# Optimization experiments

Measured on AMD Instinct MI355X. Metric: run time of the kernel, lower is better.

## Reference

```python
import jax, jax.numpy as jnp
import numpy as np

D_MODEL, H, D_FF = 512, 8, 2048
B, S = 2, 2048
EPS = 1e-6


def _layernorm(x, alpha, beta):
    # Faithful to the torch module: unbiased std (ddof=1), eps added to STD,
    # scalar alpha/beta parameters.
    m = jnp.mean(x, axis=-1, keepdims=True)
    var = jnp.sum((x - m) ** 2, axis=-1, keepdims=True) / (x.shape[-1] - 1)
    std = jnp.sqrt(var)
    return alpha * (x - m) / (std + EPS) + beta


def _mha(x, mask, Wq, bq, Wk, bk, Wv, bv, Wo, bo):
    Bn, Sn, D = x.shape
    dk = D // H
    q = (x @ Wq + bq).reshape(Bn, Sn, H, dk).transpose(0, 2, 1, 3)  # [B,H,S,dk]
    k = (x @ Wk + bk).reshape(Bn, Sn, H, dk).transpose(0, 2, 1, 3)
    v = (x @ Wv + bv).reshape(Bn, Sn, H, dk).transpose(0, 2, 1, 3)
    scores = jnp.einsum('bhqd,bhkd->bhqk', q, k) / jnp.sqrt(jnp.float32(dk))
    scores = jnp.where(mask == 0, -jnp.inf, scores)  # mask [B,1,1,S] broadcasts
    attn = jax.nn.softmax(scores, axis=-1)
    out = jnp.einsum('bhqk,bhkd->bhqd', attn, v)
    out = out.transpose(0, 2, 1, 3).reshape(Bn, Sn, D)
    return out @ Wo + bo


def _ffn(x, W1, b1, W2, b2):
    return jax.nn.relu(x @ W1 + b1) @ W2 + b2


def setup_inputs() -> dict:
    key = jax.random.key(0)
    ks = jax.random.split(key, 12)
    sd = 1.0 / np.sqrt(D_MODEL)
    sdf = 1.0 / np.sqrt(D_FF)
    inp = {
        'x': jax.random.normal(ks[0], (B, S, D_MODEL), jnp.float32),
        'src_mask': jnp.ones((B, 1, 1, S), jnp.int32),
        'Wq': jax.random.normal(ks[1], (D_MODEL, D_MODEL), jnp.float32) * sd,
        'bq': jnp.zeros((D_MODEL,), jnp.float32),
        'Wk': jax.random.normal(ks[2], (D_MODEL, D_MODEL), jnp.float32) * sd,
        'bk': jnp.zeros((D_MODEL,), jnp.float32),
        'Wv': jax.random.normal(ks[3], (D_MODEL, D_MODEL), jnp.float32) * sd,
        'bv': jnp.zeros((D_MODEL,), jnp.float32),
        'Wo': jax.random.normal(ks[4], (D_MODEL, D_MODEL), jnp.float32) * sd,
        'bo': jnp.zeros((D_MODEL,), jnp.float32),
        'W1': jax.random.normal(ks[5], (D_MODEL, D_FF), jnp.float32) * sd,
        'b1': jnp.zeros((D_FF,), jnp.float32),
        'W2': jax.random.normal(ks[6], (D_FF, D_MODEL), jnp.float32) * sdf,
        'b2': jnp.zeros((D_MODEL,), jnp.float32),
        'alpha1': jnp.ones((1,), jnp.float32),
        'beta1': jnp.zeros((1,), jnp.float32),
        'alpha2': jnp.ones((1,), jnp.float32),
        'beta2': jnp.zeros((1,), jnp.float32),
    }
    return inp


def reference(x, src_mask, Wq, bq, Wk, bk, Wv, bv, Wo, bo,
              W1, b1, W2, b2, alpha1, beta1, alpha2, beta2):
    # SkipConnection 0: x + dropout(MHA(LN(x)))  (dropout=0 -> identity)
    h1 = _layernorm(x, alpha1, beta1)
    x = x + _mha(h1, src_mask, Wq, bq, Wk, bk, Wv, bv, Wo, bo)
    # SkipConnection 1: x + dropout(FFN(LN(x)))
    h2 = _layernorm(x, alpha2, beta2)
    x = x + _ffn(h2, W1, b1, W2, b2)
    return x
```

## Files before the change

### kernel.cpp

```cpp
#include <hip/hip_runtime.h>
#include <hip/hip_bf16.h>

typedef __hip_bfloat16 bf16;
typedef __attribute__((ext_vector_type(8))) short s8v;
typedef __attribute__((ext_vector_type(4))) float f32x4;

#define DM 512
#define NH 8
#define DKH 64
#define DFF 2048
#define NB 2
#define NS 2048
#define NR (NB*NS)
#define LN_EPS 1e-6f
#define NEG_BIG (-1e30f)
#define LDQKV (3*DM)
#define SM_SCALE2 0.18033688f
#define SM_SHIFT2 (-8.656170245f)
#define PART_ELEMS (NB*NH*NS*DKH)

#define MFMA_B16(a,b,c) __builtin_amdgcn_mfma_f32_16x16x32_bf16(a,b,c,0,0,0)

#define GLOAD16(g, l) __builtin_amdgcn_global_load_lds( \
    (const __attribute__((address_space(1))) void*)(g), \
    (__attribute__((address_space(3))) void*)(l), 16, 0, 0)

__device__ __forceinline__ float us2f(unsigned int u){ return __uint_as_float(u << 16); }
__device__ __forceinline__ float b2f(bf16 v){ return __bfloat162float(v); }
__device__ __forceinline__ float ldf(const float* p){ return *p; }
__device__ __forceinline__ float ldf(const bf16* p){ return __bfloat162float(*p); }
__device__ __forceinline__ void stf(float* p, float v){ *p = v; }
__device__ __forceinline__ void stf(bf16* p, float v){ *p = __float2bfloat16(v); }

__device__ __forceinline__ int swz(int row, int colbyte){
  return ((row<<7) + colbyte) ^ ((row&7)<<4);
}

__device__ __forceinline__ float wsum(float v){
#pragma unroll
  for(int o=32;o>0;o>>=1) v += __shfl_down(v,o,64);
  return v;
}

__device__ __forceinline__ void stage_tile(char* lds, const bf16* g, int ld, int R, int tid){
  int wave = tid>>6, lane = tid&63;
  int nch = R*8;
  for(int c0 = wave*64; c0 < nch; c0 += 256){
    int c = c0 + lane;
    int row = c>>3;
    int blk = (c&7) ^ (row&7);
    GLOAD16(g + (size_t)row*ld + blk*8, lds + c0*16);
  }
}
__device__ __forceinline__ s8v read_frag(const char* lds, int row, int col){
  return *reinterpret_cast<const s8v*>(lds + swz(row, col<<1));
}

template<typename TI>
__global__ __launch_bounds__(256) void ln_kernel(const TI* __restrict__ x,
    bf16* __restrict__ out, const float* __restrict__ ap, const float* __restrict__ bp){
  __shared__ float s1[4], s2[4];
  int row = blockIdx.x, tid = threadIdx.x;
  const TI* xr = x + (size_t)row*DM;
  float v0 = ldf(xr+tid), v1 = ldf(xr+tid+256);
  float s = wsum(v0+v1);
  float q = wsum(v0*v0+v1*v1);
  int wid = tid>>6, lane = tid&63;
  if(lane==0){ s1[wid]=s; s2[wid]=q; }
  __syncthreads();
  float S = s1[0]+s1[1]+s1[2]+s1[3];
  float Q = s2[0]+s2[1]+s2[2]+s2[3];
  float mean = S*(1.f/DM);
  float var  = (Q - (float)DM*mean*mean)*(1.f/(DM-1));
  float sd   = sqrtf(fmaxf(var,0.f));
  float sc = (*ap)/(sd+LN_EPS);
  float b = *bp;
  bf16* orow = out + (size_t)row*DM;
  orow[tid]     = __float2bfloat16((v0-mean)*sc + b);
  orow[tid+256] = __float2bfloat16((v1-mean)*sc + b);
}

__global__ __launch_bounds__(256) void transpose_all(
    const float* __restrict__ Wq, const float* __restrict__ Wk,
    const float* __restrict__ Wv, const float* __restrict__ Wo,
    const float* __restrict__ W1, const float* __restrict__ W2,
    bf16* __restrict__ WTqkv, bf16* __restrict__ WTo,
    bf16* __restrict__ WT1, bf16* __restrict__ WT2){
  __shared__ float t[64][65];
  int tb = blockIdx.x;
  const float* W; bf16* WT; int K, N, nx;
  if(tb < 192){
    int w = tb>>6; tb &= 63;
    W = (w==0)?Wq:(w==1)?Wk:Wv; WT = WTqkv + w*512*512; K=512; N=512; nx=8;
  } else if(tb < 256){ tb -= 192; W=Wo; WT=WTo; K=512; N=512; nx=8; }
  else if(tb < 512){ tb -= 256; W=W1; WT=WT1; K=512; N=2048; nx=32; }
  else { tb -= 512; W=W2; WT=WT2; K=2048; N=512; nx=8; }
  int n0 = (tb % nx)*64, k0 = (tb / nx)*64;
  int tid = threadIdx.x;
  int rr = tid>>6, cc = tid&63;
#pragma unroll
  for(int r=rr;r<64;r+=4) t[r][cc] = W[(size_t)(k0+r)*N + n0+cc];
  __syncthreads();
#pragma unroll
  for(int r=rr;r<64;r+=4) WT[(size_t)(n0+r)*K + k0+cc] = __float2bfloat16(t[cc][r]);
}

__global__ __launch_bounds__(256) void transpose_v(const bf16* __restrict__ Vg,
    bf16* __restrict__ VT){
  __shared__ float t[64][65];
  int tid = threadIdx.x;
  int s0 = blockIdx.x*64; int bh = blockIdx.y;
  int b = bh>>3, h = bh&7;
  int rr = tid>>6, cc = tid&63;
#pragma unroll
  for(int r=rr;r<64;r+=4)
    t[r][cc] = b2f(Vg[((size_t)(b*NS + s0+r))*LDQKV + h*DKH + cc]);
  __syncthreads();
#pragma unroll
  for(int r=rr;r<64;r+=4)
    VT[((size_t)bh*DKH + r)*NS + s0+cc] = __float2bfloat16(t[cc][r]);
}

template<int BM, int BN, int DBUF, int RELU, int QKVSEL, typename TR, typename TO>
__global__ __launch_bounds__(256) void mfma_gemm(
    const bf16* __restrict__ A, const bf16* __restrict__ WT,
    const float* __restrict__ bias0, const float* __restrict__ bias1,
    const float* __restrict__ bias2,
    const TR* __restrict__ resid, TO* __restrict__ out, int M, int N, int K){
  constexpr int NW = BN/2, NF = NW/16, MI = BM/32, WRS = BM/2;
  __shared__ char lA[1+DBUF][BM*128];
  __shared__ char lB[1+DBUF][BN*128];
  int tid = threadIdx.x, wave = tid>>6, lane = tid&63;
  int m0 = blockIdx.x*BM, n0 = blockIdx.y*BN;
  int wr = wave>>1, wc = wave&1;
  int g = lane>>4, li = lane&15;
  f32x4 acc[MI][NF] = {};
  if(DBUF){
    stage_tile(lA[0], A + (size_t)m0*K, K, BM, tid);
    stage_tile(lB[0], WT + (size_t)n0*K, K, BN, tid);
    __syncthreads();
  }
  int cur = 0;
  for(int kt=0; kt<K; kt+=64, cur^=DBUF){
    if(!DBUF){
      stage_tile(lA[0], A + (size_t)m0*K + kt, K, BM, tid);
      stage_tile(lB[0], WT + (size_t)n0*K + kt, K, BN, tid);
      __syncthreads();
    } else if(kt+64 < K){
      stage_tile(lA[cur^1], A + (size_t)m0*K + kt+64, K, BM, tid);
      stage_tile(lB[cur^1], WT + (size_t)n0*K + kt+64, K, BN, tid);
    }
#pragma unroll
    for(int kk=0; kk<2; kk++){
      s8v af[MI], bfr[NF];
#pragma unroll
      for(int mi=0;mi<MI;mi++) af[mi] = read_frag(lA[cur], wr*WRS+mi*16+li, kk*32+g*8);
#pragma unroll
      for(int ni=0;ni<NF;ni++) bfr[ni] = read_frag(lB[cur], wc*NW+ni*16+li, kk*32+g*8);
#pragma unroll
      for(int mi=0;mi<MI;mi++)
#pragma unroll
        for(int ni=0;ni<NF;ni++)
          acc[mi][ni] = MFMA_B16(af[mi], bfr[ni], acc[mi][ni]);
    }
    __syncthreads();
  }
#pragma unroll
  for(int mi=0;mi<MI;mi++)
#pragma unroll
  for(int ni=0;ni<NF;ni++){
    int row = m0 + wr*WRS + mi*16 + g*4;
    int col = n0 + wc*NW + ni*16 + li;
    const float* bp = bias0;
    if(QKVSEL) bp = (col<512)? bias0 : (col<1024)? (bias1-512) : (bias2-1024);
    float bb = bp[col];
#pragma unroll
    for(int r=0;r<4;r++){
      float v = acc[mi][ni][r] + bb;
      if(RELU) v = fmaxf(v, 0.f);
      size_t off = (size_t)(row+r)*N + col;
      if(resid) v += ldf(resid+off);
      stf(out+off, v);
    }
  }
}

__global__ __launch_bounds__(256,4) void flash_attn(
    const bf16* __restrict__ QKV, const bf16* __restrict__ VT,
    const int* __restrict__ mask, bf16* __restrict__ partA,
    bf16* __restrict__ partB, float* __restrict__ lbuf){
  __shared__ char lK[2][64*128];
  __shared__ char lV[2][64*128];
  __shared__ char lP[4][16*128];
  int tid = threadIdx.x, wave = tid>>6, lane = tid&63;
  int q0 = blockIdx.x*64, h = blockIdx.y;
  int b = blockIdx.z>>1, kh = blockIdx.z&1;
  int kbase = kh*(NS/2);
  int g = lane>>4, li = lane&15;
  const bf16* Qg  = QKV + ((size_t)b*NS + q0)*LDQKV + h*DKH;
  const bf16* Kg  = QKV + ((size_t)b*NS + kbase)*LDQKV + DM + h*DKH;
  const bf16* VTg = VT + ((size_t)(b*NH + h))*DKH*NS + kbase;
  stage_tile(lK[0], Qg, LDQKV, 64, tid);
  __syncthreads();
  s8v qf0 = read_frag(lK[0], wave*16+li, g*8);
  s8v qf1 = read_frag(lK[0], wave*16+li, 32+g*8);
  __syncthreads();
  stage_tile(lK[0], Kg, LDQKV, 64, tid);
  stage_tile(lV[0], VTg, NS, 64, tid);
  unsigned long long mb = 0;
#pragma unroll 16
  for(int j=0;j<64;j++)
    mb |= (unsigned long long)(mask[b*NS + kbase + j*16 + li] != 0) << j;
  __syncthreads();
  f32x4 acc[4] = {};
  f32x4 acc_l = {};
  s8v ones;
#pragma unroll
  for(int j=0;j<8;j++) ones[j] = (short)0x3F80;
  char* lPw = lP[wave];
  int cur = 0;
  for(int kt=0; kt<NS/2; kt+=64, cur^=1){
    if(kt+64 < NS/2){
      stage_tile(lK[cur^1], Kg + (size_t)(kt+64)*LDQKV, LDQKV, 64, tid);
      stage_tile(lV[cur^1], VTg + kt+64, NS, 64, tid);
    }
    f32x4 S[4] = {};
#pragma unroll
    for(int kk=0;kk<2;kk++){
      s8v qf = kk ? qf1 : qf0;
      s8v kf[4];
#pragma unroll
      for(int ni=0;ni<4;ni++) kf[ni] = read_frag(lK[cur], ni*16+li, kk*32+g*8);
#pragma unroll
      for(int ni=0;ni<4;ni++)
        S[ni] = MFMA_B16(qf, kf[ni], S[ni]);
    }
    int jb = kt>>4;
    float madd[4];
#pragma unroll
    for(int ni=0;ni<4;ni++)
      madd[ni] = ((mb>>(jb+ni))&1ull) ? SM_SHIFT2 : NEG_BIG;
#pragma unroll
    for(int r=0;r<4;r++){
      float e0 = exp2f(fminf(fmaf(S[0][r], SM_SCALE2, madd[0]), 80.f));
      float e1 = exp2f(fminf(fmaf(S[1][r], SM_SCALE2, madd[1]), 80.f));
      float e2 = exp2f(fminf(fmaf(S[2][r], SM_SCALE2, madd[2]), 80.f));
      float e3 = exp2f(fminf(fmaf(S[3][r], SM_SCALE2, madd[3]), 80.f));
      int row = g*4 + r;
      *reinterpret_cast<bf16*>(lPw + swz(row, (0*16+li)<<1)) = __float2bfloat16(e0);
      *reinterpret_cast<bf16*>(lPw + swz(row, (1*16+li)<<1)) = __float2bfloat16(e1);
      *reinterpret_cast<bf16*>(lPw + swz(row, (2*16+li)<<1)) = __float2bfloat16(e2);
      *reinterpret_cast<bf16*>(lPw + swz(row, (3*16+li)<<1)) = __float2bfloat16(e3);
    }
#pragma unroll
    for(int kk=0;kk<2;kk++){
      s8v pf = read_frag(lPw, li, kk*32+g*8);
      s8v vf[4];
#pragma unroll
      for(int nd=0;nd<4;nd++) vf[nd] = read_frag(lV[cur], nd*16+li, kk*32+g*8);
#pragma unroll
      for(int nd=0;nd<4;nd++)
        acc[nd] = MFMA_B16(pf, vf[nd], acc[nd]);
      acc_l = MFMA_B16(pf, ones, acc_l);
    }
    __syncthreads();
  }
  bf16* part = kh ? partB : partA;
  size_t qb = (size_t)(b*NH + h)*NS;
#pragma unroll
  for(int r=0;r<4;r++){
    int qrow = q0 + wave*16 + g*4 + r;
#pragma unroll
    for(int nd=0;nd<4;nd++)
      part[(qb + qrow)*DKH + nd*16 + li] = __float2bfloat16(acc[nd][r]);
    if(li==0)
      lbuf[((size_t)((b*NH+h)*2 + kh))*NS + qrow] = acc_l[r];
  }
}

__global__ __launch_bounds__(256) void combine_attn(const bf16* __restrict__ pA,
    const bf16* __restrict__ pB, const float* __restrict__ lbuf,
    bf16* __restrict__ cx){
  int e = blockIdx.x*256 + threadIdx.x;
  int idx = e*4;
  int d = idx & 63, q = (idx>>6)&(NS-1), h = (idx>>17)&7, b = idx>>20;
  uint2 ua = *reinterpret_cast<const uint2*>(pA+idx);
  uint2 ub = *reinterpret_cast<const uint2*>(pB+idx);
  float lA = lbuf[((size_t)((b*NH+h)*2+0))*NS + q];
  float lB = lbuf[((size_t)((b*NH+h)*2+1))*NS + q];
  float il = 1.f/(lA+lB);
  bf16* o = cx + ((size_t)(b*NS+q)*DM + h*DKH + d);
  o[0] = __float2bfloat16((us2f(ua.x&0xffffu)+us2f(ub.x&0xffffu))*il);
  o[1] = __float2bfloat16((us2f(ua.x>>16)+us2f(ub.x>>16))*il);
  o[2] = __float2bfloat16((us2f(ua.y&0xffffu)+us2f(ub.y&0xffffu))*il);
  o[3] = __float2bfloat16((us2f(ua.y>>16)+us2f(ub.y>>16))*il);
}

extern "C" void kernel_launch(void* const* d_in, const int* in_sizes, int n_in,
                              void* d_out, int out_size, void* d_ws, size_t ws_size,
                              hipStream_t stream){
  const float* x   = (const float*)d_in[0];
  const int* mask  = (const int*)d_in[1];
  const float* Wq = (const float*)d_in[2];
  const float* bq = (const float*)d_in[3];
  const float* Wk = (const float*)d_in[4];
  const float* bk = (const float*)d_in[5];
  const float* Wv = (const float*)d_in[6];
  const float* bv = (const float*)d_in[7];
  const float* Wo = (const float*)d_in[8];
  const float* bo = (const float*)d_in[9];
  const float* W1 = (const float*)d_in[10];
  const float* b1 = (const float*)d_in[11];
  const float* W2 = (const float*)d_in[12];
  const float* b2 = (const float*)d_in[13];
  const float* a1 = (const float*)d_in[14];
  const float* be1= (const float*)d_in[15];
  const float* a2 = (const float*)d_in[16];
  const float* be2= (const float*)d_in[17];

  char* ws = (char*)d_ws;
  bf16* h1    = (bf16*)(ws);
  bf16* accA  = (bf16*)(ws);
  bf16* WTqkv = (bf16*)(ws + (size_t)( 4<<20));
  bf16* WTo   = (bf16*)(ws + (size_t)(11<<19));
  bf16* WT1   = (bf16*)(ws + (size_t)( 8<<20));
  bf16* WT2   = (bf16*)(ws + (size_t)(10<<20));
  bf16* qkv   = (bf16*)(ws + (size_t)(12<<20));
  bf16* VT    = (bf16*)(ws + (size_t)(24<<20));
  bf16* cx    = (bf16*)(ws + (size_t)(24<<20));
  bf16* x1    = h1;
  bf16* h2    = (bf16*)(ws + (size_t)( 4<<20));
  bf16* mid   = qkv;
  float* lbuf = (float*)d_out;
  bf16* accB  = (bf16*)((char*)d_out + (1<<20));

  transpose_all<<<768,256,0,stream>>>(Wq,Wk,Wv,Wo,W1,W2, WTqkv,WTo,WT1,WT2);

  ln_kernel<float><<<NR,256,0,stream>>>(x, h1, a1, be1);
  mfma_gemm<128,64,1,0,1,float,bf16><<<dim3(32,24),256,0,stream>>>(
      h1, WTqkv, bq, bk, bv, (const float*)nullptr, qkv, NR, LDQKV, DM);
  transpose_v<<<dim3(32,16),256,0,stream>>>(qkv + 2*DM, VT);
  flash_attn<<<dim3(NS/64,NH,NB*2),256,0,stream>>>(qkv, VT, mask, accA, accB, lbuf);
  combine_attn<<<PART_ELEMS/1024,256,0,stream>>>(accA, accB, lbuf, cx);
  mfma_gemm<64,64,1,0,0,float,bf16><<<dim3(64,8),256,0,stream>>>(
      cx, WTo, bo, bo, bo, x, x1, NR, DM, DM);
  ln_kernel<bf16><<<NR,256,0,stream>>>(x1, h2, a2, be2);
  mfma_gemm<128,128,0,1,0,float,bf16><<<dim3(32,16),256,0,stream>>>(
      h2, WT1, b1, b1, b1, (const float*)nullptr, mid, NR, DFF, DM);
  mfma_gemm<64,64,1,0,0,bf16,float><<<dim3(64,8),256,0,stream>>>(
      mid, WT2, b2, b2, b2, x1, (float*)d_out, NR, DM, DFF);
}
```

Baseline: 145.5 us.

## Drop split-K attention and LDS staging; load K/V fragments directly from global

The flash attention kernel no longer splits keys into two halves. It handles all 2048 keys per block and normalizes its output in place, which removes the combine kernel and the partial-output buffers. K and V fragments are read straight from global memory into registers instead of through double-buffered LDS with barriers. The QKV GEMM tile changes to 128x128, and the Wo transpose moves into a separate small kernel so its workspace can be reused. The kernel now has half as many blocks, each with a longer serial loop, and direct global fragment loads may have worse coalescing and more latency exposure. The overflow clamp on exp2 is also removed, which is only safe while the scores stay small.

```diff
diff --git a/kernel.cpp b/kernel.cpp
--- a/kernel.cpp
+++ b/kernel.cpp
@@ -17,7 +17,6 @@
 #define LDQKV (3*DM)
 #define SM_SCALE2 0.18033688f
 #define SM_SHIFT2 (-8.656170245f)
-#define PART_ELEMS (NB*NH*NS*DKH)
 
 #define MFMA_B16(a,b,c) __builtin_amdgcn_mfma_f32_16x16x32_bf16(a,b,c,0,0,0)
 
@@ -25,7 +24,6 @@
     (const __attribute__((address_space(1))) void*)(g), \
     (__attribute__((address_space(3))) void*)(l), 16, 0, 0)
 
-__device__ __forceinline__ float us2f(unsigned int u){ return __uint_as_float(u << 16); }
 __device__ __forceinline__ float b2f(bf16 v){ return __bfloat162float(v); }
 __device__ __forceinline__ float ldf(const float* p){ return *p; }
 __device__ __forceinline__ float ldf(const bf16* p){ return __bfloat162float(*p); }
@@ -82,21 +80,32 @@
 
 __global__ __launch_bounds__(256) void transpose_all(
     const float* __restrict__ Wq, const float* __restrict__ Wk,
-    const float* __restrict__ Wv, const float* __restrict__ Wo,
-    const float* __restrict__ W1, const float* __restrict__ W2,
-    bf16* __restrict__ WTqkv, bf16* __restrict__ WTo,
-    bf16* __restrict__ WT1, bf16* __restrict__ WT2){
+    const float* __restrict__ Wv, const float* __restrict__ W1,
+    const float* __restrict__ W2,
+    bf16* __restrict__ WTqkv, bf16* __restrict__ WT1, bf16* __restrict__ WT2){
   __shared__ float t[64][65];
   int tb = blockIdx.x;
   const float* W; bf16* WT; int K, N, nx;
   if(tb < 192){
     int w = tb>>6; tb &= 63;
     W = (w==0)?Wq:(w==1)?Wk:Wv; WT = WTqkv + w*512*512; K=512; N=512; nx=8;
-  } else if(tb < 256){ tb -= 192; W=Wo; WT=WTo; K=512; N=512; nx=8; }
-  else if(tb < 512){ tb -= 256; W=W1; WT=WT1; K=512; N=2048; nx=32; }
-  else { tb -= 512; W=W2; WT=WT2; K=2048; N=512; nx=8; }
+  } else if(tb < 448){ tb -= 192; W=W1; WT=WT1; K=512; N=2048; nx=32; }
+  else { tb -= 448; W=W2; WT=WT2; K=2048; N=512; nx=8; }
   int n0 = (tb % nx)*64, k0 = (tb / nx)*64;
   int tid = threadIdx.x;
+  int rr = tid>>6, cc = tid&63;
+#pragma unroll
+  for(int r=rr;r<64;r+=4) t[r][cc] = W[(size_t)(k0+r)*N + n0+cc];
+  __syncthreads();
+#pragma unroll
+  for(int r=rr;r<64;r+=4) WT[(size_t)(n0+r)*K + k0+cc] = __float2bfloat16(t[cc][r]);
+}
+
+__global__ __launch_bounds__(256) void transpose_w(const float* __restrict__ W,
+    bf16* __restrict__ WT, int K, int N){
+  __shared__ float t[64][65];
+  int tid = threadIdx.x;
+  int n0 = blockIdx.x*64, k0 = blockIdx.y*64;
   int rr = tid>>6, cc = tid&63;
 #pragma unroll
   for(int r=rr;r<64;r+=4) t[r][cc] = W[(size_t)(k0+r)*N + n0+cc];
@@ -185,67 +194,66 @@
   }
 }
 
-__global__ __launch_bounds__(256,4) void flash_attn(
+__global__ __launch_bounds__(256,3) void flash_attn(
     const bf16* __restrict__ QKV, const bf16* __restrict__ VT,
-    const int* __restrict__ mask, bf16* __restrict__ partA,
-    bf16* __restrict__ partB, float* __restrict__ lbuf){
-  __shared__ char lK[2][64*128];
-  __shared__ char lV[2][64*128];
+    const int* __restrict__ mask, bf16* __restrict__ O){
   __shared__ char lP[4][16*128];
   int tid = threadIdx.x, wave = tid>>6, lane = tid&63;
-  int q0 = blockIdx.x*64, h = blockIdx.y;
-  int b = blockIdx.z>>1, kh = blockIdx.z&1;
-  int kbase = kh*(NS/2);
+  int q0 = blockIdx.x*64, h = blockIdx.y, b = blockIdx.z;
   int g = lane>>4, li = lane&15;
   const bf16* Qg  = QKV + ((size_t)b*NS + q0)*LDQKV + h*DKH;
-  const bf16* Kg  = QKV + ((size_t)b*NS + kbase)*LDQKV + DM + h*DKH;
-  const bf16* VTg = VT + ((size_t)(b*NH + h))*DKH*NS + kbase;
-  stage_tile(lK[0], Qg, LDQKV, 64, tid);
-  __syncthreads();
-  s8v qf0 = read_frag(lK[0], wave*16+li, g*8);
-  s8v qf1 = read_frag(lK[0], wave*16+li, 32+g*8);
-  __syncthreads();
-  stage_tile(lK[0], Kg, LDQKV, 64, tid);
-  stage_tile(lV[0], VTg, NS, 64, tid);
-  unsigned long long mb = 0;
+  const bf16* Kl  = QKV + (size_t)b*NS*LDQKV + DM + h*DKH + (size_t)li*LDQKV + g*8;
+  const bf16* Vl  = VT + ((size_t)(b*NH + h))*DKH*NS + (size_t)li*NS + g*8;
+  s8v qf0 = *reinterpret_cast<const s8v*>(Qg + (size_t)(wave*16+li)*LDQKV + g*8);
+  s8v qf1 = *reinterpret_cast<const s8v*>(Qg + (size_t)(wave*16+li)*LDQKV + 32 + g*8);
+  unsigned long long mb0 = 0, mb1 = 0;
 #pragma unroll 16
   for(int j=0;j<64;j++)
-    mb |= (unsigned long long)(mask[b*NS + kbase + j*16 + li] != 0) << j;
-  __syncthreads();
+    mb0 |= (unsigned long long)(mask[b*NS + j*16 + li] != 0) << j;
+#pragma unroll 16
+  for(int j=0;j<64;j++)
+    mb1 |= (unsigned long long)(mask[b*NS + 1024 + j*16 + li] != 0) << j;
   f32x4 acc[4] = {};
   f32x4 acc_l = {};
   s8v ones;
 #pragma unroll
   for(int j=0;j<8;j++) ones[j] = (short)0x3F80;
   char* lPw = lP[wave];
-  int cur = 0;
-  for(int kt=0; kt<NS/2; kt+=64, cur^=1){
-    if(kt+64 < NS/2){
-      stage_tile(lK[cur^1], Kg + (size_t)(kt+64)*LDQKV, LDQKV, 64, tid);
-      stage_tile(lV[cur^1], VTg + kt+64, NS, 64, tid);
-    }
+  for(int kt=0; kt<NS; kt+=64){
+    const bf16* Kt = Kl + (size_t)kt*LDQKV;
+    s8v kf[2][4], vf[2][4];
+#pragma unroll
+    for(int kk=0;kk<2;kk++)
+#pragma unroll
+      for(int ni=0;ni<4;ni++)
+        kf[kk][ni] = *reinterpret_cast<const s8v*>(Kt + (size_t)(ni*16)*LDQKV + kk*32);
+#pragma unroll
+    for(int kk=0;kk<2;kk++)
+#pragma unroll
+      for(int nd=0;nd<4;nd++)
+        vf[kk][nd] = *reinterpret_cast<const s8v*>(Vl + (size_t)(nd*16)*NS + kt + kk*32);
     f32x4 S[4] = {};
 #pragma unroll
     for(int kk=0;kk<2;kk++){
       s8v qf = kk ? qf1 : qf0;
-      s8v kf[4];
-#pragma unroll
-      for(int ni=0;ni<4;ni++) kf[ni] = read_frag(lK[cur], ni*16+li, kk*32+g*8);
 #pragma unroll
       for(int ni=0;ni<4;ni++)
-        S[ni] = MFMA_B16(qf, kf[ni], S[ni]);
+        S[ni] = MFMA_B16(qf, kf[kk][ni], S[ni]);
     }
     int jb = kt>>4;
     float madd[4];
 #pragma unroll
-    for(int ni=0;ni<4;ni++)
-      madd[ni] = ((mb>>(jb+ni))&1ull) ? SM_SHIFT2 : NEG_BIG;
+    for(int ni=0;ni<4;ni++){
+      int j = jb + ni;
+      unsigned long long w = (j & 64) ? mb1 : mb0;
+      madd[ni] = ((w>>(j&63))&1ull) ? SM_SHIFT2 : NEG_BIG;
+    }
 #pragma unroll
     for(int r=0;r<4;r++){
-      float e0 = exp2f(fminf(fmaf(S[0][r], SM_SCALE2, madd[0]), 80.f));
-      float e1 = exp2f(fminf(fmaf(S[1][r], SM_SCALE2, madd[1]), 80.f));
-      float e2 = exp2f(fminf(fmaf(S[2][r], SM_SCALE2, madd[2]), 80.f));
-      float e3 = exp2f(fminf(fmaf(S[3][r], SM_SCALE2, madd[3]), 80.f));
+      float e0 = exp2f(fmaf(S[0][r], SM_SCALE2, madd[0]));
+      float e1 = exp2f(fmaf(S[1][r], SM_SCALE2, madd[1]));
+      float e2 = exp2f(fmaf(S[2][r], SM_SCALE2, madd[2]));
+      float e3 = exp2f(fmaf(S[3][r], SM_SCALE2, madd[3]));
       int row = g*4 + r;
       *reinterpret_cast<bf16*>(lPw + swz(row, (0*16+li)<<1)) = __float2bfloat16(e0);
       *reinterpret_cast<bf16*>(lPw + swz(row, (1*16+li)<<1)) = __float2bfloat16(e1);
@@ -255,45 +263,21 @@
 #pragma unroll
     for(int kk=0;kk<2;kk++){
       s8v pf = read_frag(lPw, li, kk*32+g*8);
-      s8v vf[4];
-#pragma unroll
-      for(int nd=0;nd<4;nd++) vf[nd] = read_frag(lV[cur], nd*16+li, kk*32+g*8);
 #pragma unroll
       for(int nd=0;nd<4;nd++)
-        acc[nd] = MFMA_B16(pf, vf[nd], acc[nd]);
+        acc[nd] = MFMA_B16(pf, vf[kk][nd], acc[nd]);
       acc_l = MFMA_B16(pf, ones, acc_l);
     }
-    __syncthreads();
-  }
-  bf16* part = kh ? partB : partA;
-  size_t qb = (size_t)(b*NH + h)*NS;
+  }
+  size_t obase = (size_t)b*NS*DM + h*DKH;
 #pragma unroll
   for(int r=0;r<4;r++){
+    float il = 1.f/acc_l[r];
     int qrow = q0 + wave*16 + g*4 + r;
 #pragma unroll
     for(int nd=0;nd<4;nd++)
-      part[(qb + qrow)*DKH + nd*16 + li] = __float2bfloat16(acc[nd][r]);
-    if(li==0)
-      lbuf[((size_t)((b*NH+h)*2 + kh))*NS + qrow] = acc_l[r];
-  }
-}
-
-__global__ __launch_bounds__(256) void combine_attn(const bf16* __restrict__ pA,
-    const bf16* __restrict__ pB, const float* __restrict__ lbuf,
-    bf16* __restrict__ cx){
-  int e = blockIdx.x*256 + threadIdx.x;
-  int idx = e*4;
-  int d = idx & 63, q = (idx>>6)&(NS-1), h = (idx>>17)&7, b = idx>>20;
-  uint2 ua = *reinterpret_cast<const uint2*>(pA+idx);
-  uint2 ub = *reinterpret_cast<const uint2*>(pB+idx);
-  float lA = lbuf[((size_t)((b*NH+h)*2+0))*NS + q];
-  float lB = lbuf[((size_t)((b*NH+h)*2+1))*NS + q];
-  float il = 1.f/(lA+lB);
-  bf16* o = cx + ((size_t)(b*NS+q)*DM + h*DKH + d);
-  o[0] = __float2bfloat16((us2f(ua.x&0xffffu)+us2f(ub.x&0xffffu))*il);
-  o[1] = __float2bfloat16((us2f(ua.x>>16)+us2f(ub.x>>16))*il);
-  o[2] = __float2bfloat16((us2f(ua.y&0xffffu)+us2f(ub.y&0xffffu))*il);
-  o[3] = __float2bfloat16((us2f(ua.y>>16)+us2f(ub.y>>16))*il);
+      O[obase + (size_t)qrow*DM + nd*16 + li] = __float2bfloat16(acc[nd][r]*il);
+  }
 }
 
 extern "C" void kernel_launch(void* const* d_in, const int* in_sizes, int n_in,
@@ -320,28 +304,25 @@
 
   char* ws = (char*)d_ws;
   bf16* h1    = (bf16*)(ws);
-  bf16* accA  = (bf16*)(ws);
+  bf16* cx    = (bf16*)(ws);
+  bf16* h2    = (bf16*)(ws);
   bf16* WTqkv = (bf16*)(ws + (size_t)( 4<<20));
-  bf16* WTo   = (bf16*)(ws + (size_t)(11<<19));
+  bf16* x1    = (bf16*)(ws + (size_t)( 4<<20));
   bf16* WT1   = (bf16*)(ws + (size_t)( 8<<20));
   bf16* WT2   = (bf16*)(ws + (size_t)(10<<20));
   bf16* qkv   = (bf16*)(ws + (size_t)(12<<20));
+  bf16* mid   = (bf16*)(ws + (size_t)(12<<20));
   bf16* VT    = (bf16*)(ws + (size_t)(24<<20));
-  bf16* cx    = (bf16*)(ws + (size_t)(24<<20));
-  bf16* x1    = h1;
-  bf16* h2    = (bf16*)(ws + (size_t)( 4<<20));
-  bf16* mid   = qkv;
-  float* lbuf = (float*)d_out;
-  bf16* accB  = (bf16*)((char*)d_out + (1<<20));
-
-  transpose_all<<<768,256,0,stream>>>(Wq,Wk,Wv,Wo,W1,W2, WTqkv,WTo,WT1,WT2);
+  bf16* WTo   = (bf16*)(ws + (size_t)(24<<20));
+
+  transpose_all<<<704,256,0,stream>>>(Wq,Wk,Wv,W1,W2, WTqkv,WT1,WT2);
 
   ln_kernel<float><<<NR,256,0,stream>>>(x, h1, a1, be1);
-  mfma_gemm<128,64,1,0,1,float,bf16><<<dim3(32,24),256,0,stream>>>(
+  mfma_gemm<128,128,0,0,1,float,bf16><<<dim3(32,12),256,0,stream>>>(
       h1, WTqkv, bq, bk, bv, (const float*)nullptr, qkv, NR, LDQKV, DM);
   transpose_v<<<dim3(32,16),256,0,stream>>>(qkv + 2*DM, VT);
-  flash_attn<<<dim3(NS/64,NH,NB*2),256,0,stream>>>(qkv, VT, mask, accA, accB, lbuf);
-  combine_attn<<<PART_ELEMS/1024,256,0,stream>>>(accA, accB, lbuf, cx);
+  flash_attn<<<dim3(NS/64,NH,NB),256,0,stream>>>(qkv, VT, mask, cx);
+  transpose_w<<<dim3(8,8),256,0,stream>>>(Wo, WTo, DM, DM);
   mfma_gemm<64,64,1,0,0,float,bf16><<<dim3(64,8),256,0,stream>>>(
       cx, WTo, bo, bo, bo, x, x1, NR, DM, DM);
   ln_kernel<bf16><<<NR,256,0,stream>>>(x1, h2, a2, be2);
```

Measured after the change: 222.6 us. +53.0%, slower.

## Overlap K/V tile prefetch with compute using partial vmcnt waits

Applied to the files above, without the earlier changes.

Restructures the attention key loop into a prologue-free double-buffered pipeline. The next K/V tile is issued before computing on the current one, and the code waits only with s_waitcnt vmcnt(4) on the older loads instead of a full __syncthreads drain, so global-to-LDS loads overlap the MFMA and exp work. It also drops the fminf clamp before exp2f, saving ALU work but risking overflow if scores exceed the assumed range. Correctness depends on the vmcnt count matching the number of loads stage_tile issues per call.

```diff
diff --git a/kernel.cpp b/kernel.cpp
--- a/kernel.cpp
+++ b/kernel.cpp
@@ -218,19 +218,15 @@
 #pragma unroll
   for(int j=0;j<8;j++) ones[j] = (short)0x3F80;
   char* lPw = lP[wave];
-  int cur = 0;
-  for(int kt=0; kt<NS/2; kt+=64, cur^=1){
-    if(kt+64 < NS/2){
-      stage_tile(lK[cur^1], Kg + (size_t)(kt+64)*LDQKV, LDQKV, 64, tid);
-      stage_tile(lV[cur^1], VTg + kt+64, NS, 64, tid);
-    }
+
+  auto compute = [&](int kt, int c){
     f32x4 S[4] = {};
 #pragma unroll
     for(int kk=0;kk<2;kk++){
       s8v qf = kk ? qf1 : qf0;
       s8v kf[4];
 #pragma unroll
-      for(int ni=0;ni<4;ni++) kf[ni] = read_frag(lK[cur], ni*16+li, kk*32+g*8);
+      for(int ni=0;ni<4;ni++) kf[ni] = read_frag(lK[c], ni*16+li, kk*32+g*8);
 #pragma unroll
       for(int ni=0;ni<4;ni++)
         S[ni] = MFMA_B16(qf, kf[ni], S[ni]);
@@ -242,10 +238,10 @@
       madd[ni] = ((mb>>(jb+ni))&1ull) ? SM_SHIFT2 : NEG_BIG;
 #pragma unroll
     for(int r=0;r<4;r++){
-      float e0 = exp2f(fminf(fmaf(S[0][r], SM_SCALE2, madd[0]), 80.f));
-      float e1 = exp2f(fminf(fmaf(S[1][r], SM_SCALE2, madd[1]), 80.f));
-      float e2 = exp2f(fminf(fmaf(S[2][r], SM_SCALE2, madd[2]), 80.f));
-      float e3 = exp2f(fminf(fmaf(S[3][r], SM_SCALE2, madd[3]), 80.f));
+      float e0 = exp2f(fmaf(S[0][r], SM_SCALE2, madd[0]));
+      float e1 = exp2f(fmaf(S[1][r], SM_SCALE2, madd[1]));
+      float e2 = exp2f(fmaf(S[2][r], SM_SCALE2, madd[2]));
+      float e3 = exp2f(fmaf(S[3][r], SM_SCALE2, madd[3]));
       int row = g*4 + r;
       *reinterpret_cast<bf16*>(lPw + swz(row, (0*16+li)<<1)) = __float2bfloat16(e0);
       *reinterpret_cast<bf16*>(lPw + swz(row, (1*16+li)<<1)) = __float2bfloat16(e1);
@@ -257,14 +253,29 @@
       s8v pf = read_frag(lPw, li, kk*32+g*8);
       s8v vf[4];
 #pragma unroll
-      for(int nd=0;nd<4;nd++) vf[nd] = read_frag(lV[cur], nd*16+li, kk*32+g*8);
+      for(int nd=0;nd<4;nd++) vf[nd] = read_frag(lV[c], nd*16+li, kk*32+g*8);
 #pragma unroll
       for(int nd=0;nd<4;nd++)
         acc[nd] = MFMA_B16(pf, vf[nd], acc[nd]);
       acc_l = MFMA_B16(pf, ones, acc_l);
     }
-    __syncthreads();
-  }
+  };
+
+  int cur = 0;
+  for(int t=0; t<15; ++t, cur^=1){
+    stage_tile(lK[cur^1], Kg + (size_t)(t+1)*64*LDQKV, LDQKV, 64, tid);
+    stage_tile(lV[cur^1], VTg + (t+1)*64, NS, 64, tid);
+    asm volatile("s_waitcnt vmcnt(4)" ::: "memory");
+    __builtin_amdgcn_sched_barrier(0);
+    __builtin_amdgcn_s_barrier();
+    compute(t*64, cur);
+    __builtin_amdgcn_s_barrier();
+  }
+  asm volatile("s_waitcnt vmcnt(0)" ::: "memory");
+  __builtin_amdgcn_sched_barrier(0);
+  __builtin_amdgcn_s_barrier();
+  compute(15*64, cur);
+
   bf16* part = kh ? partB : partA;
   size_t qb = (size_t)(b*NH + h)*NS;
 #pragma unroll
```

New measurement: 142.7 us. No clear change (-2.0%).
